# Performance work log

Hardware: AMD Instinct MI355X
Metric: run time of the kernel (lower is better)

## Reference

```python
import jax, jax.numpy as jnp
import numpy as np

# iRPE contextual+transposed, method=PRODUCT, rpe config ratio=1.9
ALPHA, BETA, GAMMA = 1.9, 3.8, 15.2
BETA_INT = int(BETA)            # 3
S = 2 * BETA_INT + 1            # 7
NUM_BUCKETS = S * S             # 49
B, H, D = 8, 8, 64
HEIGHT = WIDTH = 32
L = HEIGHT * WIDTH              # 1024, skip = L - height*width = 0


def _piecewise_index(rp):
    # numpy port of torch piecewise_index (no-grad, precomputed constant)
    rp = np.asarray(rp)
    rp_abs = np.abs(rp)
    safe = np.maximum(rp_abs.astype(np.float64), ALPHA)  # avoid log(0) under mask
    y = ALPHA + np.log(safe / ALPHA) / np.log(GAMMA / ALPHA) * (BETA - ALPHA)
    y = np.minimum(np.round(y), BETA)                    # round then clip(max=beta)
    out = np.where(rp_abs <= ALPHA, np.round(rp.astype(np.float64)), np.sign(rp) * y)
    return out.astype(np.int64)                          # trunc toward zero (+-3.8 -> +-3)


def _rp_bucket_product(height, width):
    pos = np.stack(np.meshgrid(np.arange(height), np.arange(width), indexing='ij'), -1)
    pos = pos.reshape(-1, 2)                             # (L, 2)
    diff = pos[:, None, :] - pos[None, :, :]             # (L, L, 2)
    r = _piecewise_index(diff[:, :, 0]) + BETA_INT
    c = _piecewise_index(diff[:, :, 1]) + BETA_INT
    return (r * S + c).astype(np.int32)                  # values in [0, 49)


def setup_inputs() -> dict:
    key = jax.random.key(0)
    k1, k2 = jax.random.split(key)
    x = jax.random.normal(k1, (B, H, L, D), dtype=jnp.float32)
    lookup_table_weight = jax.random.normal(k2, (H, D, NUM_BUCKETS), dtype=jnp.float32) * 0.02
    rp_bucket = jnp.asarray(_rp_bucket_product(HEIGHT, WIDTH))  # (L, L) int32 constant
    return {"x": x, "lookup_table_weight": lookup_table_weight, "rp_bucket": rp_bucket}


def reference(x, lookup_table_weight, rp_bucket):
    # x: (B, H, L, D); lookup_table_weight: (H, D, K); rp_bucket: (L, L) int
    # lt[b,h,l,k] = sum_d x[b,h,l,d] * W[h,d,k]
    lt = jnp.einsum('bhld,hdk->bhlk', x, lookup_table_weight)  # (B, H, L, K) small
    Lq = rp_bucket.shape[0]
    row = jnp.arange(Lq)[:, None]                              # (L, 1)
    # out[b,h,i,j] = lt[b,h,i,rp_bucket[i,j]] -- the big irregular gather
    return lt[:, :, row, rp_bucket]                            # (B, H, L, L)
```

## Files before the change

kernel.cpp:

```cpp
#include <hip/hip_runtime.h>


constexpr int cL  = 1024;
constexpr int cD  = 64;
constexpr int cK  = 49;
constexpr int cIT = 8;

typedef float vf4 __attribute__((ext_vector_type(4)));

__device__ __forceinline__ int bucket_c(int d) {
    int a = d < 0 ? -d : d;
    int m = a < 4 ? a : 4;
    m -= (m >= 3) ? 1 : 0;
    int p = d < 0 ? -m : m;
    return p + 3;
}

__global__ __launch_bounds__(256) void irpe_fused_probe(
    const float* __restrict__ x,
    const float* __restrict__ W,
    float*       __restrict__ out)
{
    __shared__ vf4   xs4[cIT][cD / 4];
    __shared__ float lts[cIT * cK];

    const int gid = blockIdx.x;
    const int bh  = gid & 63;
    const int it  = gid >> 6;
    const int i0  = it * cIT;
    const int h   = bh & 7;
    const int tid = threadIdx.x;

    if (tid < cIT * (cD / 4)) {
        const int li = tid >> 4;
        const int dq = tid & 15;
        xs4[li][dq] =
            ((const vf4*)x)[((size_t)bh * cL + (i0 + li)) * (cD / 4) + dq];
    }
    __syncthreads();

    for (int p = tid; p < cIT * cK; p += 256) {
        const int li = p / cK;
        const int k  = p - li * cK;
        const float* wp = W + (size_t)h * cD * cK + k;
        const float* xr = (const float*)&xs4[li][0];
        float acc = 0.0f;
        #pragma unroll
        for (int d = 0; d < cD; ++d) acc = fmaf(xr[d], wp[(size_t)d * cK], acc);
        lts[p] = acc;
    }
    __syncthreads();

    const int j0   = tid * 4;
    const int xj   = j0 & 31;
    const int yj   = j0 >> 5;
    const int yi   = i0 >> 5;
    const int xi0  = i0 & 31;
    const int rbase = 7 * bucket_c(yi - yj);
    const int base  = xi0 - xj;
    int cv[11];
    #pragma unroll
    for (int t = 0; t < 11; ++t) cv[t] = rbase + bucket_c(base + t - 3);

    vf4* obase = (vf4*)(out + ((size_t)bh * cL + i0) * cL);
    for (int pass = 0; pass < 3; ++pass) {
        #pragma unroll
        for (int il = 0; il < cIT; ++il) {
            const float* lrow = lts + il * cK;
            vf4 o;
            o.x = lrow[cv[il + 3]];
            o.y = lrow[cv[il + 2]];
            o.z = lrow[cv[il + 1]];
            o.w = lrow[cv[il + 0]];
            obase[(size_t)il * (cL / 4) + tid] = o;
        }
        __syncthreads();
        asm volatile("" ::: "memory");
    }
}

extern "C" void kernel_launch(void* const* d_in, const int* in_sizes, int n_in,
                              void* d_out, int out_size, void* d_ws, size_t ws_size,
                              hipStream_t stream) {
    const float* x   = (const float*)d_in[0];
    const float* W   = (const float*)d_in[1];
    float*       out = (float*)d_out;

    irpe_fused_probe<<<64 * (cL / cIT), 256, 0, stream>>>(x, W, out);
}
```

Baseline: 332.1 us.

## Process 128-row segments per block with prefetched x chunks and single output pass

Each block now covers 128 query rows of one (b,h) pair, handled as 16-row chunks instead of one 8-row tile per block. The next chunk's x rows are loaded into registers while the current chunk's output is written, and the small GEMV results are double-buffered in shared memory with padded rows. The grid shrinks from 8192 to 512 blocks, which cuts per-block setup and the repeated loading of W. The earlier probe's triple rewrite of every output tile is removed, so each output value is written once. The trade-offs are fewer blocks in flight and a GEMV step that stays serial between chunks.

After: 390.5 us. 17.6% more time.

```diff
diff --git a/kernel.cpp b/kernel.cpp
--- a/kernel.cpp
+++ b/kernel.cpp
@@ -4,7 +4,10 @@
 constexpr int cL  = 1024;
 constexpr int cD  = 64;
 constexpr int cK  = 49;
-constexpr int cIT = 8;
+constexpr int cKP = 52;
+constexpr int cCH = 16;
+constexpr int cSEG = 128;
+constexpr int cNCH = cSEG / cCH;
 
 typedef float vf4 __attribute__((ext_vector_type(4)));
 
@@ -16,57 +19,70 @@
     return p + 3;
 }
 
-__global__ __launch_bounds__(256) void irpe_fused_probe(
+__device__ __forceinline__ void gemv_chunk(
+    const float* __restrict__ xsbuf,
+    float*       __restrict__ ltbuf,
+    const float* __restrict__ W, int h, int tid)
+{
+    for (int p = tid; p < cCH * cK; p += 256) {
+        const int li = p / cK;
+        const int k  = p - li * cK;
+        const float* wp = W + (size_t)h * cD * cK + k;
+        const float* xr = xsbuf + li * cD;
+        float acc = 0.0f;
+        #pragma unroll
+        for (int d = 0; d < cD; ++d)
+            acc = fmaf(xr[d], wp[(size_t)d * cK], acc);
+        ltbuf[li * cKP + k] = acc;
+    }
+}
+
+__global__ __launch_bounds__(256) void irpe_persist(
     const float* __restrict__ x,
     const float* __restrict__ W,
     float*       __restrict__ out)
 {
-    __shared__ vf4   xs4[cIT][cD / 4];
-    __shared__ float lts[cIT * cK];
+    __shared__ float xs[2][cCH * cD];
+    __shared__ float lts[2][cCH * cKP];
 
     const int gid = blockIdx.x;
     const int bh  = gid & 63;
-    const int it  = gid >> 6;
-    const int i0  = it * cIT;
+    const int seg = gid >> 6;
+    const int i0  = seg * cSEG;
     const int h   = bh & 7;
     const int tid = threadIdx.x;
 
-    if (tid < cIT * (cD / 4)) {
-        const int li = tid >> 4;
-        const int dq = tid & 15;
-        xs4[li][dq] =
-            ((const vf4*)x)[((size_t)bh * cL + (i0 + li)) * (cD / 4) + dq];
-    }
+    const int j0 = tid * 4;
+    const int xj = j0 & 31;
+    const int yj = j0 >> 5;
+
+    const vf4* xsrc = (const vf4*)(x + ((size_t)bh * cL + i0) * cD);
+
+    ((vf4*)xs[0])[tid] = xsrc[tid];
+    __syncthreads();
+    gemv_chunk(xs[0], lts[0], W, h, tid);
     __syncthreads();
 
-    for (int p = tid; p < cIT * cK; p += 256) {
-        const int li = p / cK;
-        const int k  = p - li * cK;
-        const float* wp = W + (size_t)h * cD * cK + k;
-        const float* xr = (const float*)&xs4[li][0];
-        float acc = 0.0f;
+    int cur = 0;
+    for (int c = 0; c < cNCH; ++c) {
+        vf4 xn;
+        const bool more = (c + 1 < cNCH);
+        if (more) xn = xsrc[(c + 1) * 256 + tid];
+
+        const int i0c   = i0 + c * cCH;
+        const int yi    = i0c >> 5;
+        const int xi0   = i0c & 31;
+        const int rbase = 7 * bucket_c(yi - yj);
+        int cv[cCH + 3];
         #pragma unroll
-        for (int d = 0; d < cD; ++d) acc = fmaf(xr[d], wp[(size_t)d * cK], acc);
-        lts[p] = acc;
-    }
-    __syncthreads();
+        for (int t = 0; t < cCH + 3; ++t)
+            cv[t] = rbase + bucket_c(xi0 - xj + t - 3);
 
-    const int j0   = tid * 4;
-    const int xj   = j0 & 31;
-    const int yj   = j0 >> 5;
-    const int yi   = i0 >> 5;
-    const int xi0  = i0 & 31;
-    const int rbase = 7 * bucket_c(yi - yj);
-    const int base  = xi0 - xj;
-    int cv[11];
-    #pragma unroll
-    for (int t = 0; t < 11; ++t) cv[t] = rbase + bucket_c(base + t - 3);
-
-    vf4* obase = (vf4*)(out + ((size_t)bh * cL + i0) * cL);
-    for (int pass = 0; pass < 3; ++pass) {
+        vf4* obase = (vf4*)(out + ((size_t)bh * cL + i0c) * cL);
+        const float* lbase = lts[cur];
         #pragma unroll
-        for (int il = 0; il < cIT; ++il) {
-            const float* lrow = lts + il * cK;
+        for (int il = 0; il < cCH; ++il) {
+            const float* lrow = lbase + il * cKP;
             vf4 o;
             o.x = lrow[cv[il + 3]];
             o.y = lrow[cv[il + 2]];
@@ -74,8 +90,14 @@
             o.w = lrow[cv[il + 0]];
             obase[(size_t)il * (cL / 4) + tid] = o;
         }
-        __syncthreads();
-        asm volatile("" ::: "memory");
+
+        if (more) {
+            ((vf4*)xs[cur ^ 1])[tid] = xn;
+            __syncthreads();
+            gemv_chunk(xs[cur ^ 1], lts[cur ^ 1], W, h, tid);
+            __syncthreads();
+            cur ^= 1;
+        }
     }
 }
 
@@ -86,5 +108,6 @@
     const float* W   = (const float*)d_in[1];
     float*       out = (float*)d_out;
 
-    irpe_fused_probe<<<64 * (cL / cIT), 256, 0, stream>>>(x, W, out);
+    const int grid = 64 * (cL / cSEG);
+    irpe_persist<<<grid, 256, 0, stream>>>(x, W, out);
 }
```

## Stream rows per wavefront with register-resident weights and shuffle-based gather

Applied to the files above, without the earlier changes.

Replaces the per-8-row block design with one where each wavefront owns 32 query rows. Each lane keeps one weight column (one bucket) in registers and computes that row's lookup value directly. The output gather then uses cross-lane shuffles instead of shared-memory reads. It also drops the redundant triple-write probe loop, so each output element is stored once, and the grid shrinks to 512 larger blocks. The trade-offs are heavy register use, lanes beyond the 49 buckets doing duplicate work, and lower block count that may reduce latency hiding for the store-bound output.

Result: faster. 285.9 us (median of 2 runs) (-13.9%).

```diff
diff --git a/kernel.cpp b/kernel.cpp
--- a/kernel.cpp
+++ b/kernel.cpp
@@ -1,10 +1,10 @@
 #include <hip/hip_runtime.h>
 
 
-constexpr int cL  = 1024;
-constexpr int cD  = 64;
-constexpr int cK  = 49;
-constexpr int cIT = 8;
+constexpr int cL = 1024;
+constexpr int cD = 64;
+constexpr int cK = 49;
+constexpr int cRW = 32;
 
 typedef float vf4 __attribute__((ext_vector_type(4)));
 
@@ -16,66 +16,74 @@
     return p + 3;
 }
 
-__global__ __launch_bounds__(256) void irpe_fused_probe(
+__global__ __launch_bounds__(256) void irpe_wavestream(
     const float* __restrict__ x,
     const float* __restrict__ W,
     float*       __restrict__ out)
 {
-    __shared__ vf4   xs4[cIT][cD / 4];
-    __shared__ float lts[cIT * cK];
+    __shared__ float xw[4][cRW * cD];
 
-    const int gid = blockIdx.x;
-    const int bh  = gid & 63;
-    const int it  = gid >> 6;
-    const int i0  = it * cIT;
-    const int h   = bh & 7;
-    const int tid = threadIdx.x;
+    const int gid  = blockIdx.x;
+    const int bh   = gid & 63;
+    const int segq = gid >> 6;
+    const int tid  = threadIdx.x;
+    const int w    = tid >> 6;
+    const int lane = tid & 63;
+    const int i0w  = segq * 128 + w * cRW;
+    const int h    = bh & 7;
 
-    if (tid < cIT * (cD / 4)) {
-        const int li = tid >> 4;
-        const int dq = tid & 15;
-        xs4[li][dq] =
-            ((const vf4*)x)[((size_t)bh * cL + (i0 + li)) * (cD / 4) + dq];
-    }
-    __syncthreads();
+    const int klane = lane < cK ? lane : lane - cK;
+    float wreg[cD];
+    const float* wcol = W + (size_t)h * cD * cK + klane;
+    #pragma unroll
+    for (int d = 0; d < cD; ++d) wreg[d] = wcol[(size_t)d * cK];
 
-    for (int p = tid; p < cIT * cK; p += 256) {
-        const int li = p / cK;
-        const int k  = p - li * cK;
-        const float* wp = W + (size_t)h * cD * cK + k;
-        const float* xr = (const float*)&xs4[li][0];
-        float acc = 0.0f;
+    vf4*       xw4  = (vf4*)xw[w];
+    const vf4* xsrc = (const vf4*)(x + ((size_t)bh * cL + i0w) * cD);
+    #pragma unroll
+    for (int r = 0; r < 8; ++r) xw4[r * 64 + lane] = xsrc[r * 64 + lane];
+
+    const int xj = (lane * 4) & 31;
+    const int l8 = lane >> 3;
+
+    const float* xrow  = xw[w];
+    vf4*         obase = (vf4*)(out + ((size_t)bh * cL + i0w) * cL);
+
+    for (int rp = 0; rp < cRW; rp += 2) {
+        float a0 = 0.0f, a1 = 0.0f;
+        const vf4* xr0 = (const vf4*)(xrow + (rp + 0) * cD);
+        const vf4* xr1 = (const vf4*)(xrow + (rp + 1) * cD);
         #pragma unroll
-        for (int d = 0; d < cD; ++d) acc = fmaf(xr[d], wp[(size_t)d * cK], acc);
-        lts[p] = acc;
-    }
-    __syncthreads();
-
-    const int j0   = tid * 4;
-    const int xj   = j0 & 31;
-    const int yj   = j0 >> 5;
-    const int yi   = i0 >> 5;
-    const int xi0  = i0 & 31;
-    const int rbase = 7 * bucket_c(yi - yj);
-    const int base  = xi0 - xj;
-    int cv[11];
-    #pragma unroll
-    for (int t = 0; t < 11; ++t) cv[t] = rbase + bucket_c(base + t - 3);
-
-    vf4* obase = (vf4*)(out + ((size_t)bh * cL + i0) * cL);
-    for (int pass = 0; pass < 3; ++pass) {
+        for (int dq = 0; dq < cD / 4; ++dq) {
+            vf4 v0 = xr0[dq];
+            vf4 v1 = xr1[dq];
+            #pragma unroll
+            for (int u = 0; u < 4; ++u) {
+                a0 = fmaf(v0[u], wreg[dq * 4 + u], a0);
+                a1 = fmaf(v1[u], wreg[dq * 4 + u], a1);
+            }
+        }
         #pragma unroll
-        for (int il = 0; il < cIT; ++il) {
-            const float* lrow = lts + il * cK;
-            vf4 o;
-            o.x = lrow[cv[il + 3]];
-            o.y = lrow[cv[il + 2]];
-            o.z = lrow[cv[il + 1]];
-            o.w = lrow[cv[il + 0]];
-            obase[(size_t)il * (cL / 4) + tid] = o;
+        for (int rr = 0; rr < 2; ++rr) {
+            const int   i   = i0w + rp + rr;
+            const float acc = rr ? a1 : a0;
+            const int   yi  = i >> 5;
+            const int   xi  = i & 31;
+            const int   bse = xi - xj;
+            int cb[4];
+            #pragma unroll
+            for (int cc = 0; cc < 4; ++cc) cb[cc] = bucket_c(bse - cc);
+            #pragma unroll
+            for (int s = 0; s < 4; ++s) {
+                const int rb = 7 * bucket_c(yi - (s * 8 + l8));
+                vf4 o;
+                o.x = __shfl(acc, rb + cb[0], 64);
+                o.y = __shfl(acc, rb + cb[1], 64);
+                o.z = __shfl(acc, rb + cb[2], 64);
+                o.w = __shfl(acc, rb + cb[3], 64);
+                obase[(size_t)(rp + rr) * (cL / 4) + s * 64 + lane] = o;
+            }
         }
-        __syncthreads();
-        asm volatile("" ::: "memory");
     }
 }
 
@@ -86,5 +94,6 @@
     const float* W   = (const float*)d_in[1];
     float*       out = (float*)d_out;
 
-    irpe_fused_probe<<<64 * (cL / cIT), 256, 0, stream>>>(x, W, out);
+    const int grid = 64 * 8;
+    irpe_wavestream<<<grid, 256, 0, stream>>>(x, W, out);
 }
```
